# Performance work log

Measured on AMD Instinct MI355X. Metric: run time of the kernel, lower is better.

The kernel has to match this reference:

```python
import jax, jax.numpy as jnp
import numpy as np

# dims: N batch, L seq, H heads, d projection_dim, P position_dimension
N, Lq, Lk, H, d, P = 2, 1024, 1024, 8, 64, 1
D = H * d


def _kernel(x):
    # _log_exp_kernel: positive feature map log(1+exp(x)) (softplus)
    return jax.nn.softplus(x)


def setup_inputs() -> dict:
    key = jax.random.key(0)
    ks = jax.random.split(key, 8)
    sc = 1.0 / np.sqrt(D).astype(np.float32)
    return {
        "query": jax.random.normal(ks[0], (N, Lq, D), jnp.float32),
        "key_seq": jax.random.normal(ks[1], (N, Lk, D), jnp.float32),
        "Wq": jax.random.normal(ks[2], (D, D), jnp.float32) * sc,
        "Wk": jax.random.normal(ks[3], (D, D), jnp.float32) * sc,
        "Wv": jax.random.normal(ks[4], (D, D), jnp.float32) * sc,
        "position_coeffs": jax.random.uniform(ks[5], (H, d), jnp.float32, 0.5, 1.5),
        "position_weight": jax.random.normal(ks[6], (H, d, P), jnp.float32) * 1e-3,
        "position_bias": jax.random.normal(ks[7], (H, d), jnp.float32) * 1e-2,
    }


def reference(query, key_seq, Wq, Wk, Wv, position_coeffs, position_weight, position_bias):
    # torch Linear (no bias): y = x @ W.T
    q = _kernel(jnp.einsum('nld,ed->nle', query, Wq).reshape(N, Lq, H, d))
    k = _kernel(jnp.einsum('nld,ed->nle', key_seq, Wk).reshape(N, Lk, H, d))
    v = jnp.einsum('nld,ed->nle', key_seq, Wv).reshape(N, Lk, H, d)
    # (N, H, L, d)
    q = jnp.transpose(q, (0, 2, 1, 3))
    k = jnp.transpose(k, (0, 2, 1, 3))
    v = jnp.transpose(v, (0, 2, 1, 3))

    # default positions: arange, query_offset = 0
    qpos = jnp.broadcast_to(jnp.arange(Lq, dtype=jnp.float32).reshape(1, Lq, 1), (N, Lq, P))
    kpos = jnp.broadcast_to(jnp.arange(Lk, dtype=jnp.float32).reshape(1, Lk, 1), (N, Lk, P))
    pq = jnp.einsum('nlp,hkp->nhlk', qpos, position_weight) + position_bias[None, :, None, :]
    pk = jnp.einsum('nlp,hkp->nhlk', kpos, position_weight)

    coeff = position_coeffs[None, :, None, :]  # (1, H, 1, d)

    def part(f, values):
        # causal (mask_future) linear attention via inclusive cumsum over keys
        Qf = q * f(pq) * coeff           # (N, H, Lq, d)
        Kf = k * f(pk)                   # (N, H, Lk, d)
        S = jnp.cumsum(jnp.einsum('nhkd,nhke->nhkde', Kf, values), axis=2)
        return jnp.einsum('nhqd,nhqde->nhqe', Qf, S)

    num = part(jnp.cos, v) + part(jnp.sin, v)           # (N, H, Lq, d)
    unit = jnp.ones((N, H, Lk, 1), jnp.float32)
    den = part(jnp.cos, unit) + part(jnp.sin, unit)     # (N, H, Lq, 1)
    attn = num / den
    return jnp.transpose(attn, (0, 2, 1, 3)).reshape(N, Lq, D)
```

## Files before the change

kernel.cpp:

```cpp
#include <hip/hip_runtime.h>
#include <cmath>

#define NB    2
#define LSEQ  1024
#define NH    8
#define HD    64
#define DD    512
#define FDIM  128
#define EV    65
#define SEP   80
#define CHUNK 64
#define NC    16
#define NBH   16

typedef short short8 __attribute__((ext_vector_type(8)));
typedef float floatx4 __attribute__((ext_vector_type(4)));
typedef unsigned short ushort;

__device__ __forceinline__ float softplusf(float x) {
  return fmaxf(x, 0.0f) + log1pf(expf(-fabsf(x)));
}

__device__ __forceinline__ ushort f2bf(float f) {
  unsigned u = __float_as_uint(f);
  u += 0x7fffu + ((u >> 16) & 1u);
  return (ushort)(u >> 16);
}

__device__ __forceinline__ short8 cvt8(float4 a, float4 b) {
  short8 r;
  r[0] = (short)f2bf(a.x); r[1] = (short)f2bf(a.y);
  r[2] = (short)f2bf(a.z); r[3] = (short)f2bf(a.w);
  r[4] = (short)f2bf(b.x); r[5] = (short)f2bf(b.y);
  r[6] = (short)f2bf(b.z); r[7] = (short)f2bf(b.w);
  return r;
}

__global__ __launch_bounds__(256) void k_cvt(
    const float* __restrict__ Xq, const float* __restrict__ Xkv,
    const float* __restrict__ Wq, const float* __restrict__ Wk,
    const float* __restrict__ Wv,
    ushort* __restrict__ Xqb, ushort* __restrict__ Xkvb,
    ushort* __restrict__ Wqb, ushort* __restrict__ Wkb,
    ushort* __restrict__ Wvb)
{
  const int i = blockIdx.x * 256 + threadIdx.x;
  const float* src; ushort* dst; int g;
  if (i < 131072)      { src = Xq;  dst = Xqb;  g = i; }
  else if (i < 262144) { src = Xkv; dst = Xkvb; g = i - 131072; }
  else if (i < 294912) { src = Wq;  dst = Wqb;  g = i - 262144; }
  else if (i < 327680) { src = Wk;  dst = Wkb;  g = i - 294912; }
  else                 { src = Wv;  dst = Wvb;  g = i - 327680; }
  const float4 a = ((const float4*)src)[(size_t)g * 2];
  const float4 b = ((const float4*)src)[(size_t)g * 2 + 1];
  *(short8*)&dst[(size_t)g * 8] = cvt8(a, b);
}

__global__ __launch_bounds__(256) void k_proj(
    const ushort* __restrict__ Xqb, const ushort* __restrict__ Xkvb,
    const ushort* __restrict__ Wqb, const ushort* __restrict__ Wkb,
    const ushort* __restrict__ Wvb,
    const float* __restrict__ pw, const float* __restrict__ pb,
    const float* __restrict__ pc,
    ushort* __restrict__ Qfb, ushort* __restrict__ Kfb,
    ushort* __restrict__ Vxb)
{
  __shared__ short Al[2][64][72];
  __shared__ short Bl[2][64][72];
  const int b = ((blockIdx.x & 7) * 96) + (blockIdx.x >> 3);
  int m0, e0, pmode;
  const ushort *X, *W;
  if (b < 256) {
    m0 = (b >> 3) << 6; e0 = (b & 7) << 6;
    X = Xqb; W = Wqb + (size_t)e0 * DD; pmode = 0;
  } else {
    const int bb = b - 256;
    m0 = (bb >> 4) << 6;
    const int nt = bb & 15;
    e0 = (nt & 7) << 6;
    X = Xkvb;
    if (nt < 8) { W = Wkb + (size_t)e0 * DD; pmode = 1; }
    else        { W = Wvb + (size_t)e0 * DD; pmode = 2; }
  }
  const int tid  = threadIdx.x;
  const int r    = tid >> 2;
  const int ko   = (tid & 3) << 4;
  const int wave = tid >> 6, lane = tid & 63;
  const int quad = lane >> 4, lm = lane & 15;
  const ushort* Ag = X + (size_t)(m0 + r) * DD + ko;
  const ushort* Bg = W + (size_t)r * DD + ko;

  short8 a0 = *(const short8*)(Ag);
  short8 a1 = *(const short8*)(Ag + 8);
  short8 b0 = *(const short8*)(Bg);
  short8 b1 = *(const short8*)(Bg + 8);
  *(short8*)&Al[0][r][ko]     = a0;
  *(short8*)&Al[0][r][ko + 8] = a1;
  *(short8*)&Bl[0][r][ko]     = b0;
  *(short8*)&Bl[0][r][ko + 8] = b1;
  __syncthreads();

  floatx4 acc[4] = {};
  for (int k0 = 0; k0 < DD; k0 += 64) {
    const int cur  = (k0 >> 6) & 1;
    const bool more = (k0 + 64 < DD);
    if (more) {
      a0 = *(const short8*)(Ag + k0 + 64);
      a1 = *(const short8*)(Ag + k0 + 72);
      b0 = *(const short8*)(Bg + k0 + 64);
      b1 = *(const short8*)(Bg + k0 + 72);
    }
#pragma unroll
    for (int ks = 0; ks < 2; ++ks) {
      const short8 af = *(const short8*)&Al[cur][(wave << 4) + lm][(quad << 3) + (ks << 5)];
#pragma unroll
      for (int t = 0; t < 4; ++t) {
        const short8 bf = *(const short8*)&Bl[cur][(t << 4) + lm][(quad << 3) + (ks << 5)];
        acc[t] = __builtin_amdgcn_mfma_f32_16x16x32_bf16(af, bf, acc[t], 0, 0, 0);
      }
    }
    if (more) {
      const int nxt = cur ^ 1;
      *(short8*)&Al[nxt][r][ko]     = a0;
      *(short8*)&Al[nxt][r][ko + 8] = a1;
      *(short8*)&Bl[nxt][r][ko]     = b0;
      *(short8*)&Bl[nxt][r][ko + 8] = b1;
    }
    __syncthreads();
  }
#pragma unroll
  for (int t = 0; t < 4; ++t) {
    const int e = e0 + (t << 4) + lm;
    const int h = e >> 6, jj = e & 63;
    if (pmode == 2) {
#pragma unroll
      for (int rg = 0; rg < 4; ++rg) {
        const int m = m0 + (wave << 4) + (quad << 2) + rg;
        const int n = m >> 10, l = m & 1023;
        Vxb[((size_t)(n * NH + h) * LSEQ + l) * HD + jj] = f2bf(acc[t][rg]);
      }
    } else {
      const float pwv = pw[e];
      const float pbv = (pmode == 0) ? pb[e] : 0.0f;
      const float pcv = (pmode == 0) ? pc[e] : 1.0f;
      ushort* base = (pmode == 0) ? Qfb : Kfb;
#pragma unroll
      for (int rg = 0; rg < 4; ++rg) {
        const int m = m0 + (wave << 4) + (quad << 2) + rg;
        const int n = m >> 10, l = m & 1023;
        const float v = softplusf(acc[t][rg]) * pcv;
        const float ang = fmaf((float)l, pwv, pbv);
        ushort* dst = &base[((size_t)(n * NH + h) * LSEQ + l) * FDIM + jj];
        dst[0]  = f2bf(v * __cosf(ang));
        dst[64] = f2bf(v * __sinf(ang));
      }
    }
  }
}

__global__ __launch_bounds__(256) void k_chunk_sums(
    const ushort* __restrict__ Kfb, const ushort* __restrict__ Vxb,
    float* __restrict__ S)
{
  const int blk = blockIdx.x;
  const int bh  = blk >> 5;
  const int c   = (blk >> 1) & (NC - 1);
  const int fh  = blk & 1;
  const int f0  = fh << 6;
  const int t0  = c * CHUNK;
  const int tid  = threadIdx.x;
  const int wave = tid >> 6, lane = tid & 63;
  const int quad = lane >> 4, lm = lane & 15;

  __shared__ short KT[64][72];
  __shared__ short VT[80][72];

  for (int i = tid; i < 64 * 8; i += 256) {
    const int t = i & 63, f8 = (i >> 6) << 3;
    const short8 k8 = *(const short8*)&Kfb[((size_t)bh * LSEQ + t0 + t) * FDIM + f0 + f8];
#pragma unroll
    for (int u = 0; u < 8; ++u) KT[f8 + u][t] = k8[u];
  }
  for (int i = tid; i < 64 * 8; i += 256) {
    const int t = i & 63, e8 = (i >> 6) << 3;
    const short8 v8 = *(const short8*)&Vxb[((size_t)bh * LSEQ + t0 + t) * HD + e8];
#pragma unroll
    for (int u = 0; u < 8; ++u) VT[e8 + u][t] = v8[u];
  }
  if (tid < CHUNK) VT[64][tid] = (short)0x3F80;
  __syncthreads();

  short8 aK[2];
#pragma unroll
  for (int ks = 0; ks < 2; ++ks)
    aK[ks] = *(const short8*)&KT[(wave << 4) + lm][(quad << 3) + (ks << 5)];
  floatx4 acc[5] = {};
#pragma unroll
  for (int nt = 0; nt < 5; ++nt)
#pragma unroll
    for (int ks = 0; ks < 2; ++ks) {
      const short8 bf = *(const short8*)&VT[(nt << 4) + lm][(quad << 3) + (ks << 5)];
      acc[nt] = __builtin_amdgcn_mfma_f32_16x16x32_bf16(aK[ks], bf, acc[nt], 0, 0, 0);
    }

  float* Sb = &S[(size_t)(bh * NC + c) * SEP * FDIM];
#pragma unroll
  for (int nt = 0; nt < 4; ++nt)
#pragma unroll
    for (int rg = 0; rg < 4; ++rg) {
      const int f = f0 + (wave << 4) + (quad << 2) + rg;
      Sb[((nt << 4) + lm) * FDIM + f] = acc[nt][rg];
    }
  if (lm == 0) {
#pragma unroll
    for (int rg = 0; rg < 4; ++rg) {
      const int f = f0 + (wave << 4) + (quad << 2) + rg;
      Sb[64 * FDIM + f] = acc[4][rg];
    }
  }
}

__global__ __launch_bounds__(256) void k_scan(
    const float* __restrict__ S, ushort* __restrict__ PTb)
{
  const int bh = blockIdx.x / 13;
  const int eg = blockIdx.x % 13;
  const size_t cs = (size_t)SEP * FDIM;
  const float* Sg = S + (size_t)bh * NC * cs;
  ushort* Pg = PTb + (size_t)bh * NC * cs;
  for (int i = threadIdx.x; i < 5 * FDIM; i += 256) {
    const int e = eg * 5 + (i >> 7);
    const int f = i & 127;
    const int off = e * FDIM + f;
    float v[NC];
#pragma unroll
    for (int c = 0; c < NC; ++c) v[c] = Sg[(size_t)c * cs + off];
    float s = 0.0f;
#pragma unroll
    for (int c = 0; c < NC; ++c) {
      Pg[(size_t)c * cs + off] = f2bf(s);
      s += v[c];
    }
  }
}

__global__ __launch_bounds__(256) void k_chunk_out(
    const ushort* __restrict__ Qfb, const ushort* __restrict__ Kfb,
    const ushort* __restrict__ Vxb, const ushort* __restrict__ PTb,
    float* __restrict__ Out)
{
  const int c  = blockIdx.x & (NC - 1);
  const int bh = blockIdx.x >> 4;
  const int n  = bh >> 3, h = bh & 7;
  const int t0 = c * CHUNK;
  const int tid  = threadIdx.x;
  const int wave = tid >> 6, lane = tid & 63;
  const int quad = lane >> 4, lm = lane & 15;

  __shared__ short QL[64][136];
  __shared__ short KL[64][136];
  __shared__ short ScL[64][72];
  __shared__ short PT[80][136];
  __shared__ short VT[80][72];
  __shared__ float DenL[64];

  const ushort* Qg = &Qfb[((size_t)bh * LSEQ + t0) * FDIM];
  const ushort* Kg = &Kfb[((size_t)bh * LSEQ + t0) * FDIM];
  for (int i = tid; i < 64 * 16; i += 256) {
    const int r = i >> 4, f8 = (i & 15) << 3;
    *(short8*)&QL[r][f8] = *(const short8*)&Qg[r * FDIM + f8];
    *(short8*)&KL[r][f8] = *(const short8*)&Kg[r * FDIM + f8];
  }
  {
    const ushort* Pg = &PTb[(size_t)(bh * NC + c) * SEP * FDIM];
    for (int i = tid; i < 65 * 16; i += 256) {
      const int e = i >> 4, f8 = (i & 15) << 3;
      *(short8*)&PT[e][f8] = *(const short8*)&Pg[e * FDIM + f8];
    }
  }
  for (int i = tid; i < 64 * 8; i += 256) {
    const int t = i & 63, e8 = (i >> 6) << 3;
    const short8 v8 = *(const short8*)&Vxb[((size_t)bh * LSEQ + t0 + t) * HD + e8];
#pragma unroll
    for (int u = 0; u < 8; ++u) VT[e8 + u][t] = v8[u];
  }
  if (tid < CHUNK) VT[64][tid] = (short)0x3F80;
  __syncthreads();

  short8 aQ[4];
#pragma unroll
  for (int ks = 0; ks < 4; ++ks)
    aQ[ks] = *(const short8*)&QL[(wave << 4) + lm][(quad << 3) + (ks << 5)];

  floatx4 accS[4] = {};
#pragma unroll
  for (int nt = 0; nt < 4; ++nt)
#pragma unroll
    for (int ks = 0; ks < 4; ++ks) {
      const short8 b = *(const short8*)&KL[(nt << 4) + lm][(quad << 3) + (ks << 5)];
      accS[nt] = __builtin_amdgcn_mfma_f32_16x16x32_bf16(aQ[ks], b, accS[nt], 0, 0, 0);
    }
#pragma unroll
  for (int nt = 0; nt < 4; ++nt)
#pragma unroll
    for (int rg = 0; rg < 4; ++rg) {
      const int m = (wave << 4) + (quad << 2) + rg;
      const int t = (nt << 4) + lm;
      ScL[m][t] = (short)((t <= m) ? f2bf(accS[nt][rg]) : 0);
    }

  floatx4 accN[5] = {};
#pragma unroll
  for (int nt = 0; nt < 5; ++nt)
#pragma unroll
    for (int ks = 0; ks < 4; ++ks) {
      const short8 b = *(const short8*)&PT[(nt << 4) + lm][(quad << 3) + (ks << 5)];
      accN[nt] = __builtin_amdgcn_mfma_f32_16x16x32_bf16(aQ[ks], b, accN[nt], 0, 0, 0);
    }

  short8 aS[2];
#pragma unroll
  for (int ks = 0; ks < 2; ++ks)
    aS[ks] = *(const short8*)&ScL[(wave << 4) + lm][(quad << 3) + (ks << 5)];
  floatx4 accV[5] = {};
#pragma unroll
  for (int nt = 0; nt < 5; ++nt)
#pragma unroll
    for (int ks = 0; ks < 2; ++ks) {
      const short8 b = *(const short8*)&VT[(nt << 4) + lm][(quad << 3) + (ks << 5)];
      accV[nt] = __builtin_amdgcn_mfma_f32_16x16x32_bf16(aS[ks], b, accV[nt], 0, 0, 0);
    }

  if (lm == 0) {
#pragma unroll
    for (int rg = 0; rg < 4; ++rg)
      DenL[(wave << 4) + (quad << 2) + rg] = accN[4][rg] + accV[4][rg];
  }

#pragma unroll
  for (int rg = 0; rg < 4; ++rg) {
    const int m = (wave << 4) + (quad << 2) + rg;
    const float rden = 1.0f / DenL[m];
    const int l = t0 + m;
#pragma unroll
    for (int nt = 0; nt < 4; ++nt) {
      const float val = (accN[nt][rg] + accV[nt][rg]) * rden;
      Out[((size_t)(n * LSEQ + l)) * DD + h * HD + (nt << 4) + lm] = val;
    }
  }
}

extern "C" void kernel_launch(void* const* d_in, const int* in_sizes, int n_in,
                              void* d_out, int out_size, void* d_ws, size_t ws_size,
                              hipStream_t stream) {
  (void)in_sizes; (void)n_in; (void)out_size; (void)ws_size;
  const float* query  = (const float*)d_in[0];
  const float* keyseq = (const float*)d_in[1];
  const float* Wq     = (const float*)d_in[2];
  const float* Wk     = (const float*)d_in[3];
  const float* Wv     = (const float*)d_in[4];
  const float* pc     = (const float*)d_in[5];
  const float* pw     = (const float*)d_in[6];
  const float* pb     = (const float*)d_in[7];
  float* out = (float*)d_out;

  ushort* Qfb = (ushort*)d_ws;
  ushort* Kfb = Qfb + (size_t)NBH * LSEQ * FDIM;
  ushort* Vxb = Kfb + (size_t)NBH * LSEQ * FDIM;
  float*  S   = (float*)(Vxb + (size_t)NBH * LSEQ * HD);
  ushort* PTb = (ushort*)(S + (size_t)NBH * NC * SEP * FDIM);
  ushort* Xqb  = PTb + (size_t)NBH * NC * SEP * FDIM;
  ushort* Xkvb = Xqb  + (size_t)NB * LSEQ * DD;
  ushort* Wqb  = Xkvb + (size_t)NB * LSEQ * DD;
  ushort* Wkb  = Wqb  + (size_t)DD * DD;
  ushort* Wvb  = Wkb  + (size_t)DD * DD;

  k_cvt       <<<1408,         256, 0, stream>>>(query, keyseq, Wq, Wk, Wv, Xqb, Xkvb, Wqb, Wkb, Wvb);
  k_proj      <<<768,          256, 0, stream>>>(Xqb, Xkvb, Wqb, Wkb, Wvb, pw, pb, pc, Qfb, Kfb, Vxb);
  k_chunk_sums<<<NBH * NC * 2, 256, 0, stream>>>(Kfb, Vxb, S);
  k_scan      <<<NBH * 13,     256, 0, stream>>>(S, PTb);
  k_chunk_out <<<NBH * NC,     256, 0, stream>>>(Qfb, Kfb, Vxb, PTb, out);
}
```

Baseline: 111.0 us.

## Fuse chunk-sum and scan kernels into sequential per-head loop; widen chunk_out to 512 threads

Merges k_chunk_sums and k_scan into one kernel where each block walks all 16 chunks of a head/feature-half, accumulating the running state in MFMA registers and writing the exclusive prefix directly as bf16. This drops the fp32 S buffer round trip and one launch, and it prefetches the next chunk's K/V into registers while computing. The cost is that only 32 blocks are launched, so the scan runs serially over chunks with low parallelism. k_chunk_out now uses 8 waves, split across output column tiles, with extra barriers added.

```diff
diff --git a/kernel.cpp b/kernel.cpp
--- a/kernel.cpp
+++ b/kernel.cpp
@@ -14,6 +14,7 @@
 #define NBH   16
 
 typedef short short8 __attribute__((ext_vector_type(8)));
+typedef short short4_t __attribute__((ext_vector_type(4)));
 typedef float floatx4 __attribute__((ext_vector_type(4)));
 typedef unsigned short ushort;
 
@@ -158,93 +159,79 @@
   }
 }
 
-__global__ __launch_bounds__(256) void k_chunk_sums(
+__global__ __launch_bounds__(512) void k_sums_scan(
     const ushort* __restrict__ Kfb, const ushort* __restrict__ Vxb,
-    float* __restrict__ S)
+    ushort* __restrict__ PTb)
 {
-  const int blk = blockIdx.x;
-  const int bh  = blk >> 5;
-  const int c   = (blk >> 1) & (NC - 1);
-  const int fh  = blk & 1;
-  const int f0  = fh << 6;
-  const int t0  = c * CHUNK;
+  const int bh = blockIdx.x >> 1;
+  const int fh = blockIdx.x & 1;
+  const int f0 = fh << 6;
   const int tid  = threadIdx.x;
   const int wave = tid >> 6, lane = tid & 63;
   const int quad = lane >> 4, lm = lane & 15;
+  const int wq = wave & 3, wn = wave >> 2;
 
   __shared__ short KT[64][72];
   __shared__ short VT[80][72];
 
-  for (int i = tid; i < 64 * 8; i += 256) {
-    const int t = i & 63, f8 = (i >> 6) << 3;
-    const short8 k8 = *(const short8*)&Kfb[((size_t)bh * LSEQ + t0 + t) * FDIM + f0 + f8];
-#pragma unroll
-    for (int u = 0; u < 8; ++u) KT[f8 + u][t] = k8[u];
-  }
-  for (int i = tid; i < 64 * 8; i += 256) {
-    const int t = i & 63, e8 = (i >> 6) << 3;
-    const short8 v8 = *(const short8*)&Vxb[((size_t)bh * LSEQ + t0 + t) * HD + e8];
-#pragma unroll
-    for (int u = 0; u < 8; ++u) VT[e8 + u][t] = v8[u];
-  }
-  if (tid < CHUNK) VT[64][tid] = (short)0x3F80;
-  __syncthreads();
-
-  short8 aK[2];
-#pragma unroll
-  for (int ks = 0; ks < 2; ++ks)
-    aK[ks] = *(const short8*)&KT[(wave << 4) + lm][(quad << 3) + (ks << 5)];
-  floatx4 acc[5] = {};
-#pragma unroll
-  for (int nt = 0; nt < 5; ++nt)
-#pragma unroll
-    for (int ks = 0; ks < 2; ++ks) {
-      const short8 bf = *(const short8*)&VT[(nt << 4) + lm][(quad << 3) + (ks << 5)];
-      acc[nt] = __builtin_amdgcn_mfma_f32_16x16x32_bf16(aK[ks], bf, acc[nt], 0, 0, 0);
-    }
-
-  float* Sb = &S[(size_t)(bh * NC + c) * SEP * FDIM];
-#pragma unroll
-  for (int nt = 0; nt < 4; ++nt)
-#pragma unroll
-    for (int rg = 0; rg < 4; ++rg) {
-      const int f = f0 + (wave << 4) + (quad << 2) + rg;
-      Sb[((nt << 4) + lm) * FDIM + f] = acc[nt][rg];
-    }
-  if (lm == 0) {
-#pragma unroll
-    for (int rg = 0; rg < 4; ++rg) {
-      const int f = f0 + (wave << 4) + (quad << 2) + rg;
-      Sb[64 * FDIM + f] = acc[4][rg];
-    }
-  }
-}
-
-__global__ __launch_bounds__(256) void k_scan(
-    const float* __restrict__ S, ushort* __restrict__ PTb)
-{
-  const int bh = blockIdx.x / 13;
-  const int eg = blockIdx.x % 13;
-  const size_t cs = (size_t)SEP * FDIM;
-  const float* Sg = S + (size_t)bh * NC * cs;
-  ushort* Pg = PTb + (size_t)bh * NC * cs;
-  for (int i = threadIdx.x; i < 5 * FDIM; i += 256) {
-    const int e = eg * 5 + (i >> 7);
-    const int f = i & 127;
-    const int off = e * FDIM + f;
-    float v[NC];
-#pragma unroll
-    for (int c = 0; c < NC; ++c) v[c] = Sg[(size_t)c * cs + off];
-    float s = 0.0f;
-#pragma unroll
-    for (int c = 0; c < NC; ++c) {
-      Pg[(size_t)c * cs + off] = f2bf(s);
-      s += v[c];
-    }
-  }
-}
-
-__global__ __launch_bounds__(256) void k_chunk_out(
+  if (tid < 64) VT[64][tid] = (short)0x3F80;
+  for (int i = tid; i < 15 * 64; i += 512) VT[65 + (i >> 6)][i & 63] = 0;
+
+  const int st  = tid & 63;
+  const int sf8 = (tid >> 6) << 3;
+  const ushort* Kg = &Kfb[(size_t)bh * LSEQ * FDIM + f0];
+  const ushort* Vg = &Vxb[(size_t)bh * LSEQ * HD];
+
+  short8 kr = *(const short8*)&Kg[(size_t)st * FDIM + sf8];
+  short8 vr = *(const short8*)&Vg[(size_t)st * HD + sf8];
+#pragma unroll
+  for (int u = 0; u < 8; ++u) { KT[sf8 + u][st] = kr[u]; VT[sf8 + u][st] = vr[u]; }
+  __syncthreads();
+
+  const int NT0 = wn ? 3 : 0;
+  const int NTN = wn ? 2 : 3;
+  const int fb  = f0 + (wq << 4) + (quad << 2);
+  floatx4 acc[3] = {};
+
+  for (int c = 0; c < NC; ++c) {
+    const bool more = (c + 1 < NC);
+    if (more) {
+      const int tn = (c + 1) << 6;
+      kr = *(const short8*)&Kg[(size_t)(tn + st) * FDIM + sf8];
+      vr = *(const short8*)&Vg[(size_t)(tn + st) * HD + sf8];
+    }
+    {
+      ushort* Pg = &PTb[(size_t)(bh * NC + c) * SEP * FDIM];
+#pragma unroll
+      for (int j = 0; j < 3; ++j) if (j < NTN) {
+        const int e = ((NT0 + j) << 4) + lm;
+        short4_t p;
+        p[0] = (short)f2bf(acc[j][0]); p[1] = (short)f2bf(acc[j][1]);
+        p[2] = (short)f2bf(acc[j][2]); p[3] = (short)f2bf(acc[j][3]);
+        *(short4_t*)&Pg[(size_t)e * FDIM + fb] = p;
+      }
+    }
+    short8 aK[2];
+#pragma unroll
+    for (int ks = 0; ks < 2; ++ks)
+      aK[ks] = *(const short8*)&KT[(wq << 4) + lm][(quad << 3) + (ks << 5)];
+#pragma unroll
+    for (int j = 0; j < 3; ++j) if (j < NTN)
+#pragma unroll
+      for (int ks = 0; ks < 2; ++ks) {
+        const short8 bf = *(const short8*)&VT[((NT0 + j) << 4) + lm][(quad << 3) + (ks << 5)];
+        acc[j] = __builtin_amdgcn_mfma_f32_16x16x32_bf16(aK[ks], bf, acc[j], 0, 0, 0);
+      }
+    __syncthreads();
+    if (more) {
+#pragma unroll
+      for (int u = 0; u < 8; ++u) { KT[sf8 + u][st] = kr[u]; VT[sf8 + u][st] = vr[u]; }
+      __syncthreads();
+    }
+  }
+}
+
+__global__ __launch_bounds__(512) void k_chunk_out(
     const ushort* __restrict__ Qfb, const ushort* __restrict__ Kfb,
     const ushort* __restrict__ Vxb, const ushort* __restrict__ PTb,
     float* __restrict__ Out)
@@ -256,6 +243,7 @@
   const int tid  = threadIdx.x;
   const int wave = tid >> 6, lane = tid & 63;
   const int quad = lane >> 4, lm = lane & 15;
+  const int wq = wave & 3, wn = wave >> 2;
 
   __shared__ short QL[64][136];
   __shared__ short KL[64][136];
@@ -266,19 +254,19 @@
 
   const ushort* Qg = &Qfb[((size_t)bh * LSEQ + t0) * FDIM];
   const ushort* Kg = &Kfb[((size_t)bh * LSEQ + t0) * FDIM];
-  for (int i = tid; i < 64 * 16; i += 256) {
+  for (int i = tid; i < 64 * 16; i += 512) {
     const int r = i >> 4, f8 = (i & 15) << 3;
     *(short8*)&QL[r][f8] = *(const short8*)&Qg[r * FDIM + f8];
     *(short8*)&KL[r][f8] = *(const short8*)&Kg[r * FDIM + f8];
   }
   {
     const ushort* Pg = &PTb[(size_t)(bh * NC + c) * SEP * FDIM];
-    for (int i = tid; i < 65 * 16; i += 256) {
+    for (int i = tid; i < 65 * 16; i += 512) {
       const int e = i >> 4, f8 = (i & 15) << 3;
       *(short8*)&PT[e][f8] = *(const short8*)&Pg[e * FDIM + f8];
     }
   }
-  for (int i = tid; i < 64 * 8; i += 256) {
+  for (int i = tid; i < 64 * 8; i += 512) {
     const int t = i & 63, e8 = (i >> 6) << 3;
     const short8 v8 = *(const short8*)&Vxb[((size_t)bh * LSEQ + t0 + t) * HD + e8];
 #pragma unroll
@@ -290,62 +278,68 @@
   short8 aQ[4];
 #pragma unroll
   for (int ks = 0; ks < 4; ++ks)
-    aQ[ks] = *(const short8*)&QL[(wave << 4) + lm][(quad << 3) + (ks << 5)];
-
-  floatx4 accS[4] = {};
-#pragma unroll
-  for (int nt = 0; nt < 4; ++nt)
+    aQ[ks] = *(const short8*)&QL[(wq << 4) + lm][(quad << 3) + (ks << 5)];
+
+  floatx4 accS[2] = {};
+#pragma unroll
+  for (int j = 0; j < 2; ++j)
 #pragma unroll
     for (int ks = 0; ks < 4; ++ks) {
-      const short8 b = *(const short8*)&KL[(nt << 4) + lm][(quad << 3) + (ks << 5)];
-      accS[nt] = __builtin_amdgcn_mfma_f32_16x16x32_bf16(aQ[ks], b, accS[nt], 0, 0, 0);
-    }
-#pragma unroll
-  for (int nt = 0; nt < 4; ++nt)
+      const short8 b = *(const short8*)&KL[(((wn << 1) + j) << 4) + lm][(quad << 3) + (ks << 5)];
+      accS[j] = __builtin_amdgcn_mfma_f32_16x16x32_bf16(aQ[ks], b, accS[j], 0, 0, 0);
+    }
+#pragma unroll
+  for (int j = 0; j < 2; ++j)
 #pragma unroll
     for (int rg = 0; rg < 4; ++rg) {
-      const int m = (wave << 4) + (quad << 2) + rg;
-      const int t = (nt << 4) + lm;
-      ScL[m][t] = (short)((t <= m) ? f2bf(accS[nt][rg]) : 0);
-    }
-
-  floatx4 accN[5] = {};
-#pragma unroll
-  for (int nt = 0; nt < 5; ++nt)
+      const int m = (wq << 4) + (quad << 2) + rg;
+      const int t = (((wn << 1) + j) << 4) + lm;
+      ScL[m][t] = (short)((t <= m) ? f2bf(accS[j][rg]) : 0);
+    }
+
+  const int NT0 = wn ? 3 : 0;
+  const int NTN = wn ? 2 : 3;
+  floatx4 accN[3] = {};
+#pragma unroll
+  for (int j = 0; j < 3; ++j) if (j < NTN)
 #pragma unroll
     for (int ks = 0; ks < 4; ++ks) {
-      const short8 b = *(const short8*)&PT[(nt << 4) + lm][(quad << 3) + (ks << 5)];
-      accN[nt] = __builtin_amdgcn_mfma_f32_16x16x32_bf16(aQ[ks], b, accN[nt], 0, 0, 0);
-    }
+      const short8 b = *(const short8*)&PT[((NT0 + j) << 4) + lm][(quad << 3) + (ks << 5)];
+      accN[j] = __builtin_amdgcn_mfma_f32_16x16x32_bf16(aQ[ks], b, accN[j], 0, 0, 0);
+    }
+
+  __syncthreads();
 
   short8 aS[2];
 #pragma unroll
   for (int ks = 0; ks < 2; ++ks)
-    aS[ks] = *(const short8*)&ScL[(wave << 4) + lm][(quad << 3) + (ks << 5)];
-  floatx4 accV[5] = {};
-#pragma unroll
-  for (int nt = 0; nt < 5; ++nt)
+    aS[ks] = *(const short8*)&ScL[(wq << 4) + lm][(quad << 3) + (ks << 5)];
+  floatx4 accV[3] = {};
+#pragma unroll
+  for (int j = 0; j < 3; ++j) if (j < NTN)
 #pragma unroll
     for (int ks = 0; ks < 2; ++ks) {
-      const short8 b = *(const short8*)&VT[(nt << 4) + lm][(quad << 3) + (ks << 5)];
-      accV[nt] = __builtin_amdgcn_mfma_f32_16x16x32_bf16(aS[ks], b, accV[nt], 0, 0, 0);
-    }
-
-  if (lm == 0) {
+      const short8 b = *(const short8*)&VT[((NT0 + j) << 4) + lm][(quad << 3) + (ks << 5)];
+      accV[j] = __builtin_amdgcn_mfma_f32_16x16x32_bf16(aS[ks], b, accV[j], 0, 0, 0);
+    }
+
+  if (wn == 1 && lm == 0) {
 #pragma unroll
     for (int rg = 0; rg < 4; ++rg)
-      DenL[(wave << 4) + (quad << 2) + rg] = accN[4][rg] + accV[4][rg];
-  }
-
+      DenL[(wq << 4) + (quad << 2) + rg] = accN[1][rg] + accV[1][rg];
+  }
+  __syncthreads();
+
+  const int nout = wn ? 1 : 3;
 #pragma unroll
   for (int rg = 0; rg < 4; ++rg) {
-    const int m = (wave << 4) + (quad << 2) + rg;
+    const int m = (wq << 4) + (quad << 2) + rg;
     const float rden = 1.0f / DenL[m];
     const int l = t0 + m;
 #pragma unroll
-    for (int nt = 0; nt < 4; ++nt) {
-      const float val = (accN[nt][rg] + accV[nt][rg]) * rden;
-      Out[((size_t)(n * LSEQ + l)) * DD + h * HD + (nt << 4) + lm] = val;
+    for (int j = 0; j < 3; ++j) if (j < nout) {
+      const float val = (accN[j][rg] + accV[j][rg]) * rden;
+      Out[((size_t)(n * LSEQ + l)) * DD + h * HD + ((NT0 + j) << 4) + lm] = val;
     }
   }
 }
@@ -367,17 +361,15 @@
   ushort* Qfb = (ushort*)d_ws;
   ushort* Kfb = Qfb + (size_t)NBH * LSEQ * FDIM;
   ushort* Vxb = Kfb + (size_t)NBH * LSEQ * FDIM;
-  float*  S   = (float*)(Vxb + (size_t)NBH * LSEQ * HD);
-  ushort* PTb = (ushort*)(S + (size_t)NBH * NC * SEP * FDIM);
+  ushort* PTb = Vxb + (size_t)NBH * LSEQ * HD;
   ushort* Xqb  = PTb + (size_t)NBH * NC * SEP * FDIM;
   ushort* Xkvb = Xqb  + (size_t)NB * LSEQ * DD;
   ushort* Wqb  = Xkvb + (size_t)NB * LSEQ * DD;
   ushort* Wkb  = Wqb  + (size_t)DD * DD;
   ushort* Wvb  = Wkb  + (size_t)DD * DD;
 
-  k_cvt       <<<1408,         256, 0, stream>>>(query, keyseq, Wq, Wk, Wv, Xqb, Xkvb, Wqb, Wkb, Wvb);
-  k_proj      <<<768,          256, 0, stream>>>(Xqb, Xkvb, Wqb, Wkb, Wvb, pw, pb, pc, Qfb, Kfb, Vxb);
-  k_chunk_sums<<<NBH * NC * 2, 256, 0, stream>>>(Kfb, Vxb, S);
-  k_scan      <<<NBH * 13,     256, 0, stream>>>(S, PTb);
-  k_chunk_out <<<NBH * NC,     256, 0, stream>>>(Qfb, Kfb, Vxb, PTb, out);
-}
+  k_cvt       <<<1408,     256, 0, stream>>>(query, keyseq, Wq, Wk, Wv, Xqb, Xkvb, Wqb, Wkb, Wvb);
+  k_proj      <<<768,      256, 0, stream>>>(Xqb, Xkvb, Wqb, Wkb, Wvb, pw, pb, pc, Qfb, Kfb, Vxb);
+  k_sums_scan <<<32,       512, 0, stream>>>(Kfb, Vxb, PTb);
+  k_chunk_out <<<NBH * NC, 512, 0, stream>>>(Qfb, Kfb, Vxb, PTb, out);
+}
```

Measured after the change: 119.6 us. 1.08x slower.
